# Optimization experiments

Hardware: AMD Instinct MI355X
Metric: run time of the kernel (lower is better)

The kernel has to match this reference:

```python
import jax, jax.numpy as jnp
import numpy as np

N = 100000
E = 1600000
EMBED = 128
HEADS = 8
HEAD_DIM = EMBED // HEADS
EDGE_DIM = 6


def setup_inputs() -> dict:
    key = jax.random.key(0)
    ks = jax.random.split(key, 12)
    s = 0.05
    return {
        "x": jax.random.normal(ks[0], (N, EMBED), jnp.float32),
        "edge_index": jax.random.randint(ks[1], (2, E), 0, N, dtype=jnp.int64),
        "edge_attr": jax.random.normal(ks[2], (E, EDGE_DIM), jnp.float32),
        "Wq": jax.random.normal(ks[3], (EMBED, EMBED), jnp.float32) * s,
        "Wk": jax.random.normal(ks[4], (EMBED, EMBED), jnp.float32) * s,
        "Wv": jax.random.normal(ks[5], (EMBED, EMBED), jnp.float32) * s,
        "We1": jax.random.normal(ks[6], (EDGE_DIM, EMBED), jnp.float32) * s,
        "be1": jnp.zeros((EMBED,), jnp.float32),
        "We2": jax.random.normal(ks[7], (EMBED, HEADS), jnp.float32) * s,
        "be2": jnp.zeros((HEADS,), jnp.float32),
        "Wo": jax.random.normal(ks[8], (EMBED, EMBED), jnp.float32) * s,
        "bo": jnp.zeros((EMBED,), jnp.float32),
    }


def reference(x, edge_index, edge_attr, Wq, Wk, Wv, We1, be1, We2, be2, Wo, bo):
    num_particles = x.shape[0]
    scaling = HEAD_DIM ** (-0.5)
    # node projections -> (N, H, Dh)
    Q = (x @ Wq).reshape(num_particles, HEADS, HEAD_DIM)
    K = (x @ Wk).reshape(num_particles, HEADS, HEAD_DIM)
    V = (x @ Wv).reshape(num_particles, HEADS, HEAD_DIM)
    src, tgt = edge_index[0], edge_index[1]
    # per-edge dot-product scores (E, H)
    attn_scores = jnp.einsum('ehd,ehd->eh', Q[tgt], K[src]) * scaling
    # edge bias: Linear -> exact GELU -> Linear, (E, H)
    edge_bias = jax.nn.gelu(edge_attr @ We1 + be1, approximate=False) @ We2 + be2
    attn_scores = attn_scores + edge_bias
    # segment (scatter) softmax over edges sharing a target node
    seg_max = jax.ops.segment_max(attn_scores, tgt, num_segments=num_particles)
    ex = jnp.exp(attn_scores - seg_max[tgt])
    denom = jax.ops.segment_sum(ex, tgt, num_segments=num_particles)
    attn_weights = ex / denom[tgt]
    # weighted scatter-sum of V_src -> (N, H, Dh)
    weighted_V = attn_weights[:, :, None] * V[src]
    out = jax.ops.segment_sum(weighted_V, tgt, num_segments=num_particles)
    out = out.reshape(num_particles, EMBED) @ Wo + bo
    return out, attn_weights
```

## Files before the change

### kernel.cpp

```cpp
#include <hip/hip_runtime.h>

#define N_NODES 100000
#define N_EDGES 1600000

typedef unsigned int u32;
typedef unsigned short u16;

__device__ __forceinline__ float bf2f(u16 u){ return __uint_as_float(((u32)u) << 16); }
__device__ __forceinline__ float lo16(u32 u){ return __uint_as_float(u << 16); }
__device__ __forceinline__ float hi16(u32 u){ return __uint_as_float(u & 0xffff0000u); }
__device__ __forceinline__ u32 f2bfbits(float f){
  u32 u = __float_as_uint(f);
  return (u + 0x7fffu + ((u >> 16) & 1u)) >> 16;
}

template<int DT>
__device__ __forceinline__ float ldf(const void* p, size_t i){
  if (DT) return ((const float*)p)[i];
  else    return bf2f(((const u16*)p)[i]);
}

__device__ __forceinline__ int ld_src(const int* ei, int e, int f64){
  return f64 ? ei[2*(size_t)e] : ei[e];
}
__device__ __forceinline__ int ld_tgt(const int* ei, int e, int f64){
  return f64 ? ei[2*((size_t)N_EDGES + (size_t)e)] : ei[(size_t)N_EDGES + e];
}

extern "C" __global__ void detect_kernel(const int* __restrict__ ei,
                                         const u32* __restrict__ xw,
                                         int* __restrict__ flags)
{
  if (blockIdx.x == 0 && threadIdx.x == 0) {
    int any = 0;
    #pragma unroll
    for (int i = 0; i < 32; ++i) any |= ei[2*i + 1];
    flags[0] = (any == 0) ? 1 : 0;
    int weird = 0;
    for (int i = 0; i < 256; ++i) {
      u32 w = xw[i];
      float a = lo16(w), b = hi16(w);
      if (!(fabsf(a) < 1024.f)) weird++;
      if (!(fabsf(b) < 1024.f)) weird++;
    }
    flags[1] = (weird > 0) ? 1 : 0;
  }
}

template<int DT>
__global__ __launch_bounds__(256) void qkv_gemm_t(
    const void* __restrict__ x, const void* __restrict__ Wq,
    const void* __restrict__ Wk, const void* __restrict__ Wv,
    u16* __restrict__ Q, u16* __restrict__ Kd, u16* __restrict__ Vd,
    const int* __restrict__ flags)
{
  if (flags[1] != DT) return;
  __shared__ float xs[64*129];
  const int tid = threadIdx.x;
  const int row0 = blockIdx.x * 64;
  const void* W = (blockIdx.y == 0) ? Wq : (blockIdx.y == 1) ? Wk : Wv;
  u16* Out = (blockIdx.y == 0) ? Q : (blockIdx.y == 1) ? Kd : Vd;

  if (DT) {
    const float4* xg = (const float4*)x;
    #pragma unroll
    for (int i = 0; i < 8; ++i) {
      int li = tid + i*256;
      int r = li >> 5, c4 = li & 31;
      float4 v = make_float4(0.f,0.f,0.f,0.f);
      if (row0 + r < N_NODES) v = xg[(size_t)(row0 + r)*32 + c4];
      int base = r*129 + c4*4;
      xs[base] = v.x; xs[base+1] = v.y; xs[base+2] = v.z; xs[base+3] = v.w;
    }
  } else {
    const uint4* xg = (const uint4*)x;
    #pragma unroll
    for (int i = 0; i < 4; ++i) {
      int li = tid + i*256;
      int r = li >> 4, c8 = li & 15;
      uint4 v = make_uint4(0,0,0,0);
      if (row0 + r < N_NODES) v = xg[(size_t)(row0 + r)*16 + c8];
      int base = r*129 + c8*8;
      xs[base+0]=lo16(v.x); xs[base+1]=hi16(v.x);
      xs[base+2]=lo16(v.y); xs[base+3]=hi16(v.y);
      xs[base+4]=lo16(v.z); xs[base+5]=hi16(v.z);
      xs[base+6]=lo16(v.w); xs[base+7]=hi16(v.w);
    }
  }
  __syncthreads();

  const int cg = tid & 31;
  const int r0 = (tid >> 5) * 8;
  float acc[8][4];
  #pragma unroll
  for (int i=0;i<8;++i){ acc[i][0]=0.f; acc[i][1]=0.f; acc[i][2]=0.f; acc[i][3]=0.f; }

  for (int k = 0; k < 128; ++k) {
    float4 b;
    if (DT) {
      b = ((const float4*)W)[k*32 + cg];
    } else {
      uint2 t = ((const uint2*)W)[k*32 + cg];
      b = make_float4(lo16(t.x), hi16(t.x), lo16(t.y), hi16(t.y));
    }
    #pragma unroll
    for (int i = 0; i < 8; ++i) {
      float a = xs[(r0+i)*129 + k];
      acc[i][0] += a*b.x; acc[i][1] += a*b.y; acc[i][2] += a*b.z; acc[i][3] += a*b.w;
    }
  }
  #pragma unroll
  for (int i = 0; i < 8; ++i) {
    int gr = row0 + r0 + i;
    if (gr < N_NODES) {
      u32 p0 = f2bfbits(acc[i][0]) | (f2bfbits(acc[i][1]) << 16);
      u32 p1 = f2bfbits(acc[i][2]) | (f2bfbits(acc[i][3]) << 16);
      ((uint2*)(Out + (size_t)gr*128))[cg] = make_uint2(p0, p1);
    }
  }
}

template<int DT>
__global__ __launch_bounds__(256) void bias_kernel_t(
    const void* __restrict__ ea,
    const void* __restrict__ We1, const void* __restrict__ be1,
    const void* __restrict__ We2, const void* __restrict__ be2,
    float* __restrict__ scores, const int* __restrict__ flags)
{
  if (flags[1] != DT) return;
  __shared__ __align__(16) float wpk[128][16];
  __shared__ float b2s[8];
  const int tid = threadIdx.x;
  if (tid < 128) {
    int j = tid;
    wpk[j][0] = ldf<DT>(be1, j);
    #pragma unroll
    for (int d = 0; d < 6; ++d) wpk[j][1+d] = ldf<DT>(We1, d*128 + j);
    wpk[j][7] = 0.f;
    #pragma unroll
    for (int h = 0; h < 8; ++h) wpk[j][8+h] = ldf<DT>(We2, j*8 + h);
  }
  if (tid < 8) b2s[tid] = ldf<DT>(be2, tid);
  __syncthreads();

  const int gid = blockIdx.x * 256 + tid;
  if (gid >= N_EDGES/4) return;
  const int e0 = gid * 4;

  float4 av[6];
  float* a = (float*)av;
  if (DT) {
    const float4* eg = (const float4*)ea + (size_t)gid*6;
    #pragma unroll
    for (int i = 0; i < 6; ++i) av[i] = eg[i];
  } else {
    const uint4* eg = (const uint4*)ea + (size_t)gid*3;
    uint4 v0 = eg[0], v1 = eg[1], v2 = eg[2];
    u32 d[12] = {v0.x,v0.y,v0.z,v0.w, v1.x,v1.y,v1.z,v1.w, v2.x,v2.y,v2.z,v2.w};
    #pragma unroll
    for (int idx = 0; idx < 24; ++idx)
      a[idx] = (idx & 1) ? hi16(d[idx >> 1]) : lo16(d[idx >> 1]);
  }

  float bias[4][8];
  #pragma unroll
  for (int t=0;t<4;++t)
    #pragma unroll
    for (int h=0;h<8;++h) bias[t][h] = b2s[h];

  for (int j = 0; j < 128; ++j) {
    const float4* wp = (const float4*)wpk[j];
    float4 p0 = wp[0], p1 = wp[1], p2 = wp[2], p3 = wp[3];
    #pragma unroll
    for (int t = 0; t < 4; ++t) {
      float h = p0.x + a[t*6+0]*p0.y + a[t*6+1]*p0.z + a[t*6+2]*p0.w
                     + a[t*6+3]*p1.x + a[t*6+4]*p1.y + a[t*6+5]*p1.z;
      float g = 0.5f * h * (1.0f + erff(h * 0.70710678118654752f));
      bias[t][0] += g*p2.x; bias[t][1] += g*p2.y; bias[t][2] += g*p2.z; bias[t][3] += g*p2.w;
      bias[t][4] += g*p3.x; bias[t][5] += g*p3.y; bias[t][6] += g*p3.z; bias[t][7] += g*p3.w;
    }
  }

  #pragma unroll
  for (int t = 0; t < 4; ++t) {
    float4* so = (float4*)(scores + (size_t)(e0 + t)*8);
    so[0] = make_float4(bias[t][0],bias[t][1],bias[t][2],bias[t][3]);
    so[1] = make_float4(bias[t][4],bias[t][5],bias[t][6],bias[t][7]);
  }
}

extern "C" __global__ __launch_bounds__(256) void qk_kernel(
    const int* __restrict__ ei, const u16* __restrict__ Q, const u16* __restrict__ Kd,
    float* __restrict__ scores, const int* __restrict__ flags)
{
  int i = blockIdx.x*256 + threadIdx.x;
  int e = i >> 3, h = i & 7;
  int f64 = flags[0];
  int src = ld_src(ei, e, f64);
  int tgt = ld_tgt(ei, e, f64);
  const uint4* qr = (const uint4*)(Q  + (size_t)tgt*128 + h*16);
  const uint4* kr = (const uint4*)(Kd + (size_t)src*128 + h*16);
  uint4 qa = qr[0], qb = qr[1];
  uint4 ka = kr[0], kb = kr[1];
  float s = 0.f;
  s += lo16(qa.x)*lo16(ka.x) + hi16(qa.x)*hi16(ka.x);
  s += lo16(qa.y)*lo16(ka.y) + hi16(qa.y)*hi16(ka.y);
  s += lo16(qa.z)*lo16(ka.z) + hi16(qa.z)*hi16(ka.z);
  s += lo16(qa.w)*lo16(ka.w) + hi16(qa.w)*hi16(ka.w);
  s += lo16(qb.x)*lo16(kb.x) + hi16(qb.x)*hi16(kb.x);
  s += lo16(qb.y)*lo16(kb.y) + hi16(qb.y)*hi16(kb.y);
  s += lo16(qb.z)*lo16(kb.z) + hi16(qb.z)*hi16(kb.z);
  s += lo16(qb.w)*lo16(kb.w) + hi16(qb.w)*hi16(kb.w);
  scores[i] += s * 0.25f;
}

extern "C" __global__ __launch_bounds__(256) void hist_kernel(
    const int* __restrict__ ei, int* __restrict__ offs, const int* __restrict__ flags)
{
  int e = blockIdx.x*256 + threadIdx.x;
  if (e >= N_EDGES) return;
  int t = ld_tgt(ei, e, flags[0]);
  atomicAdd(&offs[t], 1);
}

extern "C" __global__ __launch_bounds__(1024) void scan1_kernel(
    int* __restrict__ offs, int* __restrict__ bsums)
{
  __shared__ int tmp[1024];
  int tid = threadIdx.x;
  int i = blockIdx.x*1024 + tid;
  int v = (i < N_NODES) ? offs[i] : 0;
  tmp[tid] = v;
  __syncthreads();
  for (int d = 1; d < 1024; d <<= 1) {
    int t = (tid >= d) ? tmp[tid-d] : 0;
    __syncthreads();
    tmp[tid] += t;
    __syncthreads();
  }
  if (i < N_NODES) offs[i] = tmp[tid] - v;
  if (tid == 1023) bsums[blockIdx.x] = tmp[1023];
}

extern "C" __global__ void scan2_kernel(int* __restrict__ bsums, int nb)
{
  if (threadIdx.x == 0 && blockIdx.x == 0) {
    int run = 0;
    for (int i = 0; i < nb; ++i) { int t = bsums[i]; bsums[i] = run; run += t; }
  }
}

extern "C" __global__ __launch_bounds__(1024) void scan3_kernel(
    int* __restrict__ offs, const int* __restrict__ bsums)
{
  int i = blockIdx.x*1024 + threadIdx.x;
  if (i < N_NODES) offs[i] += bsums[blockIdx.x];
}

extern "C" __global__ __launch_bounds__(256) void fill_kernel(
    const int* __restrict__ ei, int* __restrict__ offs,
    int* __restrict__ edge_sorted, const int* __restrict__ flags)
{
  int e = blockIdx.x*256 + threadIdx.x;
  if (e >= N_EDGES) return;
  int t = ld_tgt(ei, e, flags[0]);
  int p = atomicAdd(&offs[t], 1);
  edge_sorted[p] = e;
}

extern "C" __global__ __launch_bounds__(256) void node_softmax_kernel(
    const int* __restrict__ ei, const int* __restrict__ offs_incl,
    const int* __restrict__ edge_sorted, const float* __restrict__ scores,
    const u16* __restrict__ Vd, void* __restrict__ dout,
    const int* __restrict__ flags)
{
  const int wid  = threadIdx.x >> 6;
  const int lane = threadIdx.x & 63;
  const int n = blockIdx.x*4 + wid;
  if (n >= N_NODES) return;
  const int f64 = flags[0], dt = flags[1];
  const int start = (n == 0) ? 0 : offs_incl[n-1];
  const int deg = offs_incl[n] - start;
  size_t slot = dt ? ((size_t)n*128 + lane) : ((size_t)n*64 + lane);
  if (deg == 0) { ((u32*)dout)[slot] = 0; return; }
  const int h = lane >> 3, j = lane & 7;
  const int srcl = h * 8;

  float m = -3.0e38f, s = 0.f;
  for (int jj = j; jj < deg; jj += 8) {
    int e = edge_sorted[start + jj];
    float v = scores[(size_t)e*8 + h];
    float mn = fmaxf(m, v);
    s = s * __expf(m - mn) + __expf(v - mn);
    m = mn;
  }
  #pragma unroll
  for (int d = 1; d < 8; d <<= 1) {
    float mo = __shfl_xor(m, d);
    float so = __shfl_xor(s, d);
    float mn = fmaxf(m, mo);
    s = s * __expf(m - mn) + so * __expf(mo - mn);
    m = mn;
  }
  float rsum = 1.f / s;

  float acc0 = 0.f, acc1 = 0.f;
  const size_t attn_base = (size_t)N_NODES*128;
  const int nch = (deg + 7) >> 3;
  for (int c = 0; c < nch; ++c) {
    int jj = c*8 + j;
    int ee = edge_sorted[start + (jj < deg ? jj : 0)];
    float w = 0.f;
    if (jj < deg) {
      w = __expf(scores[(size_t)ee*8 + h] - m) * rsum;
      if (dt) ((float*)dout)[attn_base + (size_t)ee*8 + h] = w;
      else    ((u16*)dout)[attn_base + (size_t)ee*8 + h] = (u16)f2bfbits(w);
    }
    int s_own = ld_src(ei, ee, f64);
    int lim = deg - c*8; if (lim > 8) lim = 8;
    u32 vreg[8];
    #pragma unroll
    for (int t = 0; t < 8; ++t) {
      if (t < lim) {
        int s2 = __shfl(s_own, srcl + t);
        vreg[t] = *(const u32*)(Vd + (size_t)s2*128 + lane*2);
      }
    }
    #pragma unroll
    for (int t = 0; t < 8; ++t) {
      if (t < lim) {
        float wv = __shfl(w, srcl + t);
        acc0 += wv * lo16(vreg[t]);
        acc1 += wv * hi16(vreg[t]);
      }
    }
  }
  ((u32*)dout)[slot] = f2bfbits(acc0) | (f2bfbits(acc1) << 16);
}

template<int DT>
__global__ __launch_bounds__(256) void out_proj_t(
    const void* __restrict__ Wo, const void* __restrict__ bo,
    void* __restrict__ dout, const int* __restrict__ flags)
{
  if (flags[1] != DT) return;
  __shared__ float as_[64*129];
  const int tid = threadIdx.x;
  const int row0 = blockIdx.x * 64;
  {
    #pragma unroll
    for (int i = 0; i < 4; ++i) {
      int li = tid + i*256;
      int r = li >> 4, q = li & 15;
      int gr = row0 + r;
      uint4 v = make_uint4(0,0,0,0);
      if (gr < N_NODES) {
        const uint4* rp = (const uint4*)((const u32*)dout + (DT ? (size_t)gr*128 : (size_t)gr*64));
        v = rp[q];
      }
      int base = r*129 + q*8;
      as_[base+0]=lo16(v.x); as_[base+1]=hi16(v.x);
      as_[base+2]=lo16(v.y); as_[base+3]=hi16(v.y);
      as_[base+4]=lo16(v.z); as_[base+5]=hi16(v.z);
      as_[base+6]=lo16(v.w); as_[base+7]=hi16(v.w);
    }
  }
  __syncthreads();
  const int cg = tid & 31;
  const int r0 = (tid >> 5) * 8;
  float acc[8][4];
  #pragma unroll
  for (int i=0;i<8;++i){ acc[i][0]=0.f; acc[i][1]=0.f; acc[i][2]=0.f; acc[i][3]=0.f; }

  for (int k = 0; k < 128; ++k) {
    float4 b;
    if (DT) {
      b = ((const float4*)Wo)[k*32 + cg];
    } else {
      uint2 t = ((const uint2*)Wo)[k*32 + cg];
      b = make_float4(lo16(t.x), hi16(t.x), lo16(t.y), hi16(t.y));
    }
    #pragma unroll
    for (int i = 0; i < 8; ++i) {
      float a = as_[(r0+i)*129 + k];
      acc[i][0] += a*b.x; acc[i][1] += a*b.y; acc[i][2] += a*b.z; acc[i][3] += a*b.w;
    }
  }
  float bb0 = ldf<DT>(bo, cg*4+0), bb1 = ldf<DT>(bo, cg*4+1);
  float bb2 = ldf<DT>(bo, cg*4+2), bb3 = ldf<DT>(bo, cg*4+3);
  #pragma unroll
  for (int i = 0; i < 8; ++i) {
    int gr = row0 + r0 + i;
    if (gr < N_NODES) {
      if (DT) {
        ((float4*)((float*)dout + (size_t)gr*128))[cg] =
            make_float4(acc[i][0]+bb0, acc[i][1]+bb1, acc[i][2]+bb2, acc[i][3]+bb3);
      } else {
        u32 p0 = f2bfbits(acc[i][0]+bb0) | (f2bfbits(acc[i][1]+bb1) << 16);
        u32 p1 = f2bfbits(acc[i][2]+bb2) | (f2bfbits(acc[i][3]+bb3) << 16);
        ((uint2*)((u16*)dout + (size_t)gr*128))[cg] = make_uint2(p0, p1);
      }
    }
  }
}

extern "C" void kernel_launch(void* const* d_in, const int* in_sizes, int n_in,
                              void* d_out, int out_size, void* d_ws, size_t ws_size,
                              hipStream_t stream)
{
  const void* x   = d_in[0];
  const int*  ei  = (const int*)d_in[1];
  const void* ea  = d_in[2];
  const void* Wq  = d_in[3];
  const void* Wk  = d_in[4];
  const void* Wv  = d_in[5];
  const void* We1 = d_in[6];
  const void* be1 = d_in[7];
  const void* We2 = d_in[8];
  const void* be2 = d_in[9];
  const void* Wo  = d_in[10];
  const void* bo  = d_in[11];

  char* ws = (char*)d_ws;
  int*   flags       = (int*)  ws;
  u16*   Vd          = (u16*)  (ws + 4096);
  float* scores      = (float*)(ws + 25604096);
  int*   offs        = (int*)  (ws + 76804096);
  int*   bsums       = (int*)  (ws + 77204096);
  int*   edge_sorted = (int*)  (ws + 77204992);

  u16* Q  = (u16*)d_out;
  u16* Kd = Q + (size_t)N_NODES*128;

  detect_kernel<<<dim3(1), 64, 0, stream>>>(ei, (const u32*)x, flags);
  hipMemsetAsync(offs, 0, 400000, stream);

  qkv_gemm_t<0><<<dim3(1563,3), 256, 0, stream>>>(x, Wq, Wk, Wv, Q, Kd, Vd, flags);
  qkv_gemm_t<1><<<dim3(1563,3), 256, 0, stream>>>(x, Wq, Wk, Wv, Q, Kd, Vd, flags);

  bias_kernel_t<0><<<dim3(1563), 256, 0, stream>>>(ea, We1, be1, We2, be2, scores, flags);
  bias_kernel_t<1><<<dim3(1563), 256, 0, stream>>>(ea, We1, be1, We2, be2, scores, flags);
  qk_kernel<<<dim3(50000), 256, 0, stream>>>(ei, Q, Kd, scores, flags);

  hist_kernel <<<dim3(6250), 256, 0, stream>>>(ei, offs, flags);
  scan1_kernel<<<dim3(98), 1024, 0, stream>>>(offs, bsums);
  scan2_kernel<<<dim3(1), 64, 0, stream>>>(bsums, 98);
  scan3_kernel<<<dim3(98), 1024, 0, stream>>>(offs, bsums);
  fill_kernel <<<dim3(6250), 256, 0, stream>>>(ei, offs, edge_sorted, flags);

  node_softmax_kernel<<<dim3(25000), 256, 0, stream>>>(ei, offs, edge_sorted, scores, Vd, d_out, flags);

  out_proj_t<0><<<dim3(1563), 256, 0, stream>>>(Wo, bo, d_out, flags);
  out_proj_t<1><<<dim3(1563), 256, 0, stream>>>(Wo, bo, d_out, flags);
}
```

Measured before the change: 1.048 ms.

## Fuse QK dot product into per-node softmax, split gather into separate kernel

Removes the per-edge qk_kernel and computes Q·K scores inside a new per-target-node kernel. That kernel loads the node's Q row once, gathers K for each incoming edge, does an online softmax and writes the normalized weights. Scores for up to 64 edges per node are cached in LDS so K is not re-gathered on the second pass. A second node kernel then reads the weights and does the V gather/accumulate. This saves the redundant per-edge Q gathers and a read-modify-write pass over scores, at the cost of an extra node-level launch and a second pass over edge_sorted and src indices.

```diff
diff --git a/kernel.cpp b/kernel.cpp
--- a/kernel.cpp
+++ b/kernel.cpp
@@ -2,6 +2,7 @@
 
 #define N_NODES 100000
 #define N_EDGES 1600000
+#define MAXD 64
 
 typedef unsigned int u32;
 typedef unsigned short u16;
@@ -25,6 +26,19 @@
 }
 __device__ __forceinline__ int ld_tgt(const int* ei, int e, int f64){
   return f64 ? ei[2*((size_t)N_EDGES + (size_t)e)] : ei[(size_t)N_EDGES + e];
+}
+
+__device__ __forceinline__ float bfdot16(uint4 qa, uint4 qb, uint4 ka, uint4 kb){
+  float s = 0.f;
+  s += lo16(qa.x)*lo16(ka.x) + hi16(qa.x)*hi16(ka.x);
+  s += lo16(qa.y)*lo16(ka.y) + hi16(qa.y)*hi16(ka.y);
+  s += lo16(qa.z)*lo16(ka.z) + hi16(qa.z)*hi16(ka.z);
+  s += lo16(qa.w)*lo16(ka.w) + hi16(qa.w)*hi16(ka.w);
+  s += lo16(qb.x)*lo16(kb.x) + hi16(qb.x)*hi16(kb.x);
+  s += lo16(qb.y)*lo16(kb.y) + hi16(qb.y)*hi16(kb.y);
+  s += lo16(qb.z)*lo16(kb.z) + hi16(qb.z)*hi16(kb.z);
+  s += lo16(qb.w)*lo16(kb.w) + hi16(qb.w)*hi16(kb.w);
+  return s;
 }
 
 extern "C" __global__ void detect_kernel(const int* __restrict__ ei,
@@ -187,31 +201,6 @@
     so[0] = make_float4(bias[t][0],bias[t][1],bias[t][2],bias[t][3]);
     so[1] = make_float4(bias[t][4],bias[t][5],bias[t][6],bias[t][7]);
   }
-}
-
-extern "C" __global__ __launch_bounds__(256) void qk_kernel(
-    const int* __restrict__ ei, const u16* __restrict__ Q, const u16* __restrict__ Kd,
-    float* __restrict__ scores, const int* __restrict__ flags)
-{
-  int i = blockIdx.x*256 + threadIdx.x;
-  int e = i >> 3, h = i & 7;
-  int f64 = flags[0];
-  int src = ld_src(ei, e, f64);
-  int tgt = ld_tgt(ei, e, f64);
-  const uint4* qr = (const uint4*)(Q  + (size_t)tgt*128 + h*16);
-  const uint4* kr = (const uint4*)(Kd + (size_t)src*128 + h*16);
-  uint4 qa = qr[0], qb = qr[1];
-  uint4 ka = kr[0], kb = kr[1];
-  float s = 0.f;
-  s += lo16(qa.x)*lo16(ka.x) + hi16(qa.x)*hi16(ka.x);
-  s += lo16(qa.y)*lo16(ka.y) + hi16(qa.y)*hi16(ka.y);
-  s += lo16(qa.z)*lo16(ka.z) + hi16(qa.z)*hi16(ka.z);
-  s += lo16(qa.w)*lo16(ka.w) + hi16(qa.w)*hi16(ka.w);
-  s += lo16(qb.x)*lo16(kb.x) + hi16(qb.x)*hi16(kb.x);
-  s += lo16(qb.y)*lo16(kb.y) + hi16(qb.y)*hi16(kb.y);
-  s += lo16(qb.z)*lo16(kb.z) + hi16(qb.z)*hi16(kb.z);
-  s += lo16(qb.w)*lo16(kb.w) + hi16(qb.w)*hi16(kb.w);
-  scores[i] += s * 0.25f;
 }
 
 extern "C" __global__ __launch_bounds__(256) void hist_kernel(
@@ -268,7 +257,70 @@
   edge_sorted[p] = e;
 }
 
-extern "C" __global__ __launch_bounds__(256) void node_softmax_kernel(
+extern "C" __global__ __launch_bounds__(256) void node_score_kernel(
+    const int* __restrict__ ei, const int* __restrict__ offs_incl,
+    const int* __restrict__ edge_sorted, float* __restrict__ scores,
+    const u16* __restrict__ Q, const u16* __restrict__ Kd,
+    void* __restrict__ dout, const int* __restrict__ flags)
+{
+  __shared__ float s_lds[4][MAXD*8];
+  __shared__ int   e_lds[4][MAXD];
+  const int wid  = threadIdx.x >> 6;
+  const int lane = threadIdx.x & 63;
+  const int n = blockIdx.x*4 + wid;
+  if (n >= N_NODES) return;
+  const int f64 = flags[0], dt = flags[1];
+  const int start = (n == 0) ? 0 : offs_incl[n-1];
+  const int deg = offs_incl[n] - start;
+  if (deg == 0) return;
+  const int h = lane & 7, j = lane >> 3;
+
+  const uint4* qr = (const uint4*)(Q + (size_t)n*128 + h*16);
+  uint4 qa = qr[0], qb = qr[1];
+
+  float m = -3.0e38f, s = 0.f;
+  for (int jj = j; jj < deg; jj += 8) {
+    int e = edge_sorted[start + jj];
+    int src = ld_src(ei, e, f64);
+    const uint4* kr = (const uint4*)(Kd + (size_t)src*128 + h*16);
+    uint4 ka = kr[0], kb = kr[1];
+    float v = bfdot16(qa, qb, ka, kb) * 0.25f + scores[(size_t)e*8 + h];
+    if (jj < MAXD) {
+      s_lds[wid][jj*8 + h] = v;
+      if (h == 0) e_lds[wid][jj] = e;
+    }
+    float mn = fmaxf(m, v);
+    s = s * __expf(m - mn) + __expf(v - mn);
+    m = mn;
+  }
+  #pragma unroll
+  for (int d = 8; d < 64; d <<= 1) {
+    float mo = __shfl_xor(m, d);
+    float so = __shfl_xor(s, d);
+    float mn = fmaxf(m, mo);
+    s = s * __expf(m - mn) + so * __expf(mo - mn);
+    m = mn;
+  }
+  const float rsum = 1.f / s;
+
+  float* wout = dt ? ((float*)dout + (size_t)N_NODES*128) : scores;
+  for (int jj = j; jj < deg; jj += 8) {
+    float sv; int eo;
+    if (jj < MAXD) {
+      sv = s_lds[wid][jj*8 + h];
+      eo = e_lds[wid][jj];
+    } else {
+      eo = edge_sorted[start + jj];
+      int src = ld_src(ei, eo, f64);
+      const uint4* kr = (const uint4*)(Kd + (size_t)src*128 + h*16);
+      uint4 ka = kr[0], kb = kr[1];
+      sv = bfdot16(qa, qb, ka, kb) * 0.25f + scores[(size_t)eo*8 + h];
+    }
+    wout[(size_t)eo*8 + h] = __expf(sv - m) * rsum;
+  }
+}
+
+extern "C" __global__ __launch_bounds__(256) void node_gather_kernel(
     const int* __restrict__ ei, const int* __restrict__ offs_incl,
     const int* __restrict__ edge_sorted, const float* __restrict__ scores,
     const u16* __restrict__ Vd, void* __restrict__ dout,
@@ -283,53 +335,36 @@
   const int deg = offs_incl[n] - start;
   size_t slot = dt ? ((size_t)n*128 + lane) : ((size_t)n*64 + lane);
   if (deg == 0) { ((u32*)dout)[slot] = 0; return; }
-  const int h = lane >> 3, j = lane & 7;
-  const int srcl = h * 8;
-
-  float m = -3.0e38f, s = 0.f;
-  for (int jj = j; jj < deg; jj += 8) {
-    int e = edge_sorted[start + jj];
-    float v = scores[(size_t)e*8 + h];
-    float mn = fmaxf(m, v);
-    s = s * __expf(m - mn) + __expf(v - mn);
-    m = mn;
-  }
-  #pragma unroll
-  for (int d = 1; d < 8; d <<= 1) {
-    float mo = __shfl_xor(m, d);
-    float so = __shfl_xor(s, d);
-    float mn = fmaxf(m, mo);
-    s = s * __expf(m - mn) + so * __expf(mo - mn);
-    m = mn;
-  }
-  float rsum = 1.f / s;
+  const int h2 = lane & 7;
+  const int t0 = lane >> 3;
+  const int hC = lane >> 3;
+  const float* wsrc = dt ? ((const float*)dout + (size_t)N_NODES*128) : scores;
+  const size_t attn_b16 = (size_t)N_NODES*128;
 
   float acc0 = 0.f, acc1 = 0.f;
-  const size_t attn_base = (size_t)N_NODES*128;
   const int nch = (deg + 7) >> 3;
   for (int c = 0; c < nch; ++c) {
-    int jj = c*8 + j;
-    int ee = edge_sorted[start + (jj < deg ? jj : 0)];
-    float w = 0.f;
+    int jj = c*8 + t0;
+    float w = 0.f; int sown = 0;
     if (jj < deg) {
-      w = __expf(scores[(size_t)ee*8 + h] - m) * rsum;
-      if (dt) ((float*)dout)[attn_base + (size_t)ee*8 + h] = w;
-      else    ((u16*)dout)[attn_base + (size_t)ee*8 + h] = (u16)f2bfbits(w);
-    }
-    int s_own = ld_src(ei, ee, f64);
+      int e = edge_sorted[start + jj];
+      sown = ld_src(ei, e, f64);
+      w = wsrc[(size_t)e*8 + h2];
+      if (!dt) ((u16*)dout)[attn_b16 + (size_t)e*8 + h2] = (u16)f2bfbits(w);
+    }
     int lim = deg - c*8; if (lim > 8) lim = 8;
     u32 vreg[8];
     #pragma unroll
     for (int t = 0; t < 8; ++t) {
       if (t < lim) {
-        int s2 = __shfl(s_own, srcl + t);
+        int s2 = __shfl(sown, t*8);
         vreg[t] = *(const u32*)(Vd + (size_t)s2*128 + lane*2);
       }
     }
     #pragma unroll
     for (int t = 0; t < 8; ++t) {
       if (t < lim) {
-        float wv = __shfl(w, srcl + t);
+        float wv = __shfl(w, t*8 + hC);
         acc0 += wv * lo16(vreg[t]);
         acc1 += wv * hi16(vreg[t]);
       }
@@ -440,7 +475,6 @@
 
   bias_kernel_t<0><<<dim3(1563), 256, 0, stream>>>(ea, We1, be1, We2, be2, scores, flags);
   bias_kernel_t<1><<<dim3(1563), 256, 0, stream>>>(ea, We1, be1, We2, be2, scores, flags);
-  qk_kernel<<<dim3(50000), 256, 0, stream>>>(ei, Q, Kd, scores, flags);
 
   hist_kernel <<<dim3(6250), 256, 0, stream>>>(ei, offs, flags);
   scan1_kernel<<<dim3(98), 1024, 0, stream>>>(offs, bsums);
@@ -448,7 +482,8 @@
   scan3_kernel<<<dim3(98), 1024, 0, stream>>>(offs, bsums);
   fill_kernel <<<dim3(6250), 256, 0, stream>>>(ei, offs, edge_sorted, flags);
 
-  node_softmax_kernel<<<dim3(25000), 256, 0, stream>>>(ei, offs, edge_sorted, scores, Vd, d_out, flags);
+  node_score_kernel <<<dim3(25000), 256, 0, stream>>>(ei, offs, edge_sorted, scores, Q, Kd, d_out, flags);
+  node_gather_kernel<<<dim3(25000), 256, 0, stream>>>(ei, offs, edge_sorted, scores, Vd, d_out, flags);
 
   out_proj_t<0><<<dim3(1563), 256, 0, stream>>>(Wo, bo, d_out, flags);
   out_proj_t<1><<<dim3(1563), 256, 0, stream>>>(Wo, bo, d_out, flags);
```

Result: faster. 989.4 us (-5.6%).
